# Performance work log

Hardware: AMD Instinct MI355X
Metric: run time of the kernel (lower is better)

The kernel has to match this reference:

```python
import jax, jax.numpy as jnp
import numpy as np

MARGIN = 0.35


def setup_inputs() -> dict:
    key = jax.random.key(0)
    k1, k2 = jax.random.split(key)
    N, D = 8192, 512
    inp = jax.random.normal(k1, (N, D), dtype=jnp.float32)
    label = jax.random.randint(k2, (N,), 0, D, dtype=jnp.int64)
    return {"input": inp, "label": label}


def reference(input, label):
    N = input.shape[0]
    # Faithful to the torch code: squared-norm terms use L2-normalized input,
    # but the -2*x@x.T cross term uses the UNnormalized input (original quirk).
    x_norm = input / jnp.linalg.norm(input, axis=1, keepdims=True)
    sq = jnp.sum(x_norm * x_norm, axis=1, keepdims=True)  # [N,1]
    dist = sq + sq.T - 2.0 * (input @ input.T)            # [N,N]
    mask = label[:, None] == label[None, :]               # same-label mask
    neg_inf = jnp.array(-jnp.inf, dist.dtype)
    pos_inf = jnp.array(jnp.inf, dist.dtype)
    # hardest positive (max over same-label), hardest negative (min over diff-label)
    positive_part = jnp.max(jnp.where(mask, dist, neg_inf), axis=1)
    negative_part = jnp.min(jnp.where(mask, pos_inf, dist), axis=1)
    triplet = jnp.mean(jnp.maximum(positive_part - negative_part + MARGIN, 0.0))
    # cross entropy: input are logits, label class indices
    logz = jax.nn.logsumexp(input, axis=1)
    true_logit = jnp.take_along_axis(input, label[:, None].astype(jnp.int32), axis=1)[:, 0]
    ce = jnp.mean(logz - true_logit)
    return triplet + ce
```

## Files before the change

kernel.cpp:

```cpp
#include <hip/hip_runtime.h>
#include <hip/hip_bf16.h>
#include <stdint.h>

#define N_ROWS 8192
#define DIM 512
#define NLAB 512
#define MARGIN_F 0.35f
#define NBLK 64
#define NPURE 1953
#define NDIAG 127
#define NTILE (NPURE + NDIAG)
#define ROWSTAT_BLOCKS (N_ROWS / 4)

typedef __attribute__((ext_vector_type(4))) float floatx4;
typedef __attribute__((ext_vector_type(8))) __bf16 bf16x8;

__device__ __forceinline__ unsigned enc_f(float f) {
    unsigned u = __float_as_uint(f);
    return (u & 0x80000000u) ? ~u : (u | 0x80000000u);
}
__device__ __forceinline__ float dec_f(unsigned e) {
    unsigned u = (e & 0x80000000u) ? (e ^ 0x80000000u) : ~e;
    return __uint_as_float(u);
}

__device__ __forceinline__ void load_lds16(const void* g, void* l) {
    __builtin_amdgcn_global_load_lds((__attribute__((address_space(1))) void*)(void*)g,
                                     (__attribute__((address_space(3))) void*)l, 16, 0, 0);
}

__global__ __launch_bounds__(512) void histscan_kernel(const int* __restrict__ label,
                                                       int* __restrict__ offsetArr,
                                                       int* __restrict__ cnt,
                                                       float* __restrict__ out) {
    __shared__ int h[NLAB];
    __shared__ int sc[NLAB];
    int t = threadIdx.x;
    h[t] = 0;
    __syncthreads();
    for (int i = t; i < N_ROWS; i += 512) atomicAdd(&h[label[i]], 1);
    __syncthreads();
    int v = h[t];
    sc[t] = v;
    __syncthreads();
    for (int d = 1; d < NLAB; d <<= 1) {
        int add = (t >= d) ? sc[t - d] : 0;
        __syncthreads();
        sc[t] += add;
        __syncthreads();
    }
    offsetArr[t] = sc[t] - v;
    cnt[t] = 0;
    if (t == 0) out[0] = 0.f;
}

__global__ __launch_bounds__(256) void rowstats_kernel(const float* __restrict__ x,
                                                       const int* __restrict__ label,
                                                       const int* __restrict__ offsetArr,
                                                       int* __restrict__ cnt,
                                                       __bf16* __restrict__ abf,
                                                       int* __restrict__ sortedLabel,
                                                       float* __restrict__ cePartial,
                                                       unsigned* __restrict__ minEnc,
                                                       unsigned* __restrict__ maxEnc) {
    int gid = blockIdx.x * 256 + threadIdx.x;
    if (gid < N_ROWS) { minEnc[gid] = 0xFFFFFFFFu; maxEnc[gid] = 0u; }

    int w = threadIdx.x >> 6;
    int row = blockIdx.x * 4 + w;
    int l = threadIdx.x & 63;
    const float* xr = x + (size_t)row * DIM;
    float4 v0 = ((const float4*)xr)[2 * l];
    float4 v1 = ((const float4*)xr)[2 * l + 1];
    float vals[8] = {v0.x, v0.y, v0.z, v0.w, v1.x, v1.y, v1.z, v1.w};

    float mx = vals[0];
#pragma unroll
    for (int i = 1; i < 8; i++) mx = fmaxf(mx, vals[i]);
#pragma unroll
    for (int s = 1; s < 64; s <<= 1) mx = fmaxf(mx, __shfl_xor(mx, s, 64));

    float se = 0.f;
#pragma unroll
    for (int i = 0; i < 8; i++) se += expf(vals[i] - mx);
#pragma unroll
    for (int s = 1; s < 64; s <<= 1) se += __shfl_xor(se, s, 64);

    int pos = 0;
    if (l == 0) {
        int lab = label[row];
        pos = offsetArr[lab] + atomicAdd(&cnt[lab], 1);
        sortedLabel[pos] = lab;
    }
    pos = __shfl(pos, 0, 64);

    unsigned hp[4];
#pragma unroll
    for (int i = 0; i < 4; i++) {
        unsigned u0 = __float_as_uint(vals[2 * i]);
        u0 += 0x7FFFu + ((u0 >> 16) & 1u);
        unsigned u1 = __float_as_uint(vals[2 * i + 1]);
        u1 += 0x7FFFu + ((u1 >> 16) & 1u);
        hp[i] = (u0 >> 16) | (u1 & 0xFFFF0000u);
    }
    ((uint4*)(abf + (size_t)pos * DIM))[l] = make_uint4(hp[0], hp[1], hp[2], hp[3]);

    __shared__ float wsum[4];
    if (l == 0) {
        float tl = xr[label[row]];
        wsum[w] = mx + logf(se) - tl;
    }
    __syncthreads();
    if (threadIdx.x == 0)
        cePartial[blockIdx.x] = wsum[0] + wsum[1] + wsum[2] + wsum[3];
}

__global__ __launch_bounds__(256, 4) void gemm_kernel(const __bf16* __restrict__ A,
                                                      const int* __restrict__ sortedLabel,
                                                      unsigned* __restrict__ minEnc,
                                                      unsigned* __restrict__ maxEnc) {
    __shared__ __bf16 As[128 * 64];
    __shared__ __bf16 Bs[128 * 64];
    __shared__ float redA[128][2], redB[128][2];

    int b = blockIdx.x;
    bool diag = (b < NDIAG);
    int bi, bj;
    if (diag) {
        bi = (b < 64) ? b : (b - 63);
        bj = (b < 64) ? b : (b - 64);
    } else {
        int p = b - NDIAG;
        int ci = (int)((sqrtf(8.0f * (float)p + 1.0f) - 1.0f) * 0.5f);
        while ((ci + 1) * (ci + 2) / 2 <= p) ci++;
        while (ci * (ci + 1) / 2 > p) ci--;
        bj = p - ci * (ci + 1) / 2;
        bi = ci + 2;
    }
    int ibase = bi * 128, jbase = bj * 128;

    int t = threadIdx.x;
    int w = t >> 6, l = t & 63;
    int wm = w >> 1, wn = w & 1;
    int q = l >> 4, lm = l & 15;

    floatx4 acc[4][4];
#pragma unroll
    for (int a = 0; a < 4; a++)
#pragma unroll
        for (int c = 0; c < 4; c++) acc[a][c] = (floatx4)0.f;

    for (int kk = 0; kk < 8; kk++) {
        int k0 = kk * 64;
#pragma unroll
        for (int i2 = 0; i2 < 4; i2++) {
            int s = i2 * 256 + t;
            int r = s >> 3;
            int cg = (s & 7) ^ (r & 7);
            load_lds16(A + (size_t)(ibase + r) * DIM + k0 + cg * 8, As + s * 8);
            load_lds16(A + (size_t)(jbase + r) * DIM + k0 + cg * 8, Bs + s * 8);
        }
        __syncthreads();

#pragma unroll
        for (int ks = 0; ks < 2; ks++) {
            bf16x8 af[4], bfv[4];
#pragma unroll
            for (int tm = 0; tm < 4; tm++) {
                int R = wm * 64 + tm * 16 + lm;
                af[tm] = *(const bf16x8*)(As + R * 64 + (((ks * 4 + q) ^ (R & 7)) * 8));
            }
#pragma unroll
            for (int tn = 0; tn < 4; tn++) {
                int R = wn * 64 + tn * 16 + lm;
                bfv[tn] = *(const bf16x8*)(Bs + R * 64 + (((ks * 4 + q) ^ (R & 7)) * 8));
            }
#pragma unroll
            for (int tm = 0; tm < 4; tm++)
#pragma unroll
                for (int tn = 0; tn < 4; tn++)
                    acc[tm][tn] = __builtin_amdgcn_mfma_f32_16x16x32_bf16(af[tm], bfv[tn], acc[tm][tn], 0, 0, 0);
        }
        __syncthreads();
    }

    const float INF = __builtin_inff();

    if (!diag) {
        float mxJ[4];
#pragma unroll
        for (int tn = 0; tn < 4; tn++) mxJ[tn] = -INF;
#pragma unroll
        for (int tm = 0; tm < 4; tm++) {
#pragma unroll
            for (int r = 0; r < 4; r++) {
                int row_l = wm * 64 + tm * 16 + q * 4 + r;
                float mxI = -INF;
#pragma unroll
                for (int tn = 0; tn < 4; tn++) {
                    float v = acc[tm][tn][r];
                    mxI = fmaxf(mxI, v);
                    mxJ[tn] = fmaxf(mxJ[tn], v);
                }
#pragma unroll
                for (int s = 1; s < 16; s <<= 1)
                    mxI = fmaxf(mxI, __shfl_xor(mxI, s, 64));
                if (lm == 0) redA[row_l][wn] = mxI;
            }
        }
#pragma unroll
        for (int tn = 0; tn < 4; tn++) {
#pragma unroll
            for (int s = 16; s < 64; s <<= 1)
                mxJ[tn] = fmaxf(mxJ[tn], __shfl_xor(mxJ[tn], s, 64));
            if (q == 0) redB[wn * 64 + tn * 16 + lm][wm] = mxJ[tn];
        }
        __syncthreads();
        if (t < 128) {
            atomicMax(&maxEnc[ibase + t], enc_f(fmaxf(redA[t][0], redA[t][1])));
            atomicMax(&maxEnc[jbase + t], enc_f(fmaxf(redB[t][0], redB[t][1])));
        }
    } else {
        int* labi = (int*)As;
        int* labj = labi + 128;
        float (*redImn)[2] = (float (*)[2])(labj + 128);
        float (*redJmn)[2] = redImn + 128;
        if (t < 128) labi[t] = sortedLabel[ibase + t];
        else labj[t - 128] = sortedLabel[jbase + t - 128];
        __syncthreads();

        int jlab[4];
#pragma unroll
        for (int tn = 0; tn < 4; tn++) jlab[tn] = labj[wn * 64 + tn * 16 + lm];

        float mnJ[4], mxJ[4];
#pragma unroll
        for (int tn = 0; tn < 4; tn++) { mnJ[tn] = INF; mxJ[tn] = -INF; }

#pragma unroll
        for (int tm = 0; tm < 4; tm++) {
#pragma unroll
            for (int r = 0; r < 4; r++) {
                int row_l = wm * 64 + tm * 16 + q * 4 + r;
                int il = labi[row_l];
                float mnI = INF, mxI = -INF;
#pragma unroll
                for (int tn = 0; tn < 4; tn++) {
                    float v = acc[tm][tn][r];
                    bool same = (jlab[tn] == il);
                    float vs = same ? v : INF;
                    float vd = same ? -INF : v;
                    mnI = fminf(mnI, vs);
                    mxI = fmaxf(mxI, vd);
                    mnJ[tn] = fminf(mnJ[tn], vs);
                    mxJ[tn] = fmaxf(mxJ[tn], vd);
                }
#pragma unroll
                for (int s = 1; s < 16; s <<= 1) {
                    mnI = fminf(mnI, __shfl_xor(mnI, s, 64));
                    mxI = fmaxf(mxI, __shfl_xor(mxI, s, 64));
                }
                if (lm == 0) { redImn[row_l][wn] = mnI; redA[row_l][wn] = mxI; }
            }
        }
#pragma unroll
        for (int tn = 0; tn < 4; tn++) {
#pragma unroll
            for (int s = 16; s < 64; s <<= 1) {
                mnJ[tn] = fminf(mnJ[tn], __shfl_xor(mnJ[tn], s, 64));
                mxJ[tn] = fmaxf(mxJ[tn], __shfl_xor(mxJ[tn], s, 64));
            }
            if (q == 0) {
                int col_l = wn * 64 + tn * 16 + lm;
                redJmn[col_l][wm] = mnJ[tn];
                redB[col_l][wm] = mxJ[tn];
            }
        }
        __syncthreads();
        if (t < 128) {
            atomicMin(&minEnc[ibase + t], enc_f(fminf(redImn[t][0], redImn[t][1])));
            atomicMax(&maxEnc[ibase + t], enc_f(fmaxf(redA[t][0], redA[t][1])));
            atomicMin(&minEnc[jbase + t], enc_f(fminf(redJmn[t][0], redJmn[t][1])));
            atomicMax(&maxEnc[jbase + t], enc_f(fmaxf(redB[t][0], redB[t][1])));
        }
    }
}

__global__ __launch_bounds__(256) void finalize_kernel(const unsigned* __restrict__ minEnc,
                                                       const unsigned* __restrict__ maxEnc,
                                                       const float* __restrict__ cePartial,
                                                       float* __restrict__ out) {
    int gid = blockIdx.x * 256 + threadIdx.x;
    float mn = dec_f(minEnc[gid]);
    float mxv = dec_f(maxEnc[gid]);
    float s = fmaxf(2.0f * (mxv - mn) + MARGIN_F, 0.f);
    if (gid < ROWSTAT_BLOCKS) s += cePartial[gid];
#pragma unroll
    for (int sh = 1; sh < 64; sh <<= 1) s += __shfl_xor(s, sh, 64);
    __shared__ float red[4];
    int w = threadIdx.x >> 6, l = threadIdx.x & 63;
    if (l == 0) red[w] = s;
    __syncthreads();
    if (threadIdx.x == 0)
        atomicAdd(out, (red[0] + red[1] + red[2] + red[3]) * (1.0f / (float)N_ROWS));
}

extern "C" void kernel_launch(void* const* d_in, const int* in_sizes, int n_in,
                              void* d_out, int out_size, void* d_ws, size_t ws_size,
                              hipStream_t stream) {
    const float* x = (const float*)d_in[0];
    const int* label = (const int*)d_in[1];
    float* out = (float*)d_out;

    char* ws = (char*)d_ws;
    __bf16* abf = (__bf16*)ws;
    char* p = ws + (size_t)N_ROWS * DIM * 2;
    unsigned* minEnc = (unsigned*)p;            p += N_ROWS * 4;
    unsigned* maxEnc = (unsigned*)p;            p += N_ROWS * 4;
    float* cePartial = (float*)p;               p += ROWSTAT_BLOCKS * 4;
    int* offsetArr = (int*)p;                   p += NLAB * 4;
    int* cnt = (int*)p;                         p += NLAB * 4;
    int* sortedLabel = (int*)p;                 p += N_ROWS * 4;

    histscan_kernel<<<1, 512, 0, stream>>>(label, offsetArr, cnt, out);
    rowstats_kernel<<<ROWSTAT_BLOCKS, 256, 0, stream>>>(x, label, offsetArr, cnt, abf,
                                                        sortedLabel, cePartial, minEnc, maxEnc);
    gemm_kernel<<<NTILE, 256, 0, stream>>>(abf, sortedLabel, minEnc, maxEnc);
    finalize_kernel<<<32, 256, 0, stream>>>(minEnc, maxEnc, cePartial, out);
}
```

Measured before the change: 125.9 us.

## Switch distance GEMM from bf16 to fp8 with scaled 16x16x128 MFMA

Rowstats now quantizes input rows to fp8 e4m3 instead of bf16, and the GEMM kernel uses the f8f6f4 scaled MFMA with K=128 per instruction, so there are half as many K iterations. LDS tiles hold 128 bytes per row, keeping the same XOR swizzle. This halves the global and LDS traffic and doubles matrix throughput per instruction. The trade-off is that fp8 precision can distort the hardest positive/negative distances and move the loss outside tolerance.

```diff
diff --git a/kernel.cpp b/kernel.cpp
--- a/kernel.cpp
+++ b/kernel.cpp
@@ -13,7 +13,7 @@
 #define ROWSTAT_BLOCKS (N_ROWS / 4)
 
 typedef __attribute__((ext_vector_type(4))) float floatx4;
-typedef __attribute__((ext_vector_type(8))) __bf16 bf16x8;
+typedef __attribute__((ext_vector_type(8))) int intx8;
 
 __device__ __forceinline__ unsigned enc_f(float f) {
     unsigned u = __float_as_uint(f);
@@ -58,7 +58,7 @@
                                                        const int* __restrict__ label,
                                                        const int* __restrict__ offsetArr,
                                                        int* __restrict__ cnt,
-                                                       __bf16* __restrict__ abf,
+                                                       unsigned char* __restrict__ a8,
                                                        int* __restrict__ sortedLabel,
                                                        float* __restrict__ cePartial,
                                                        unsigned* __restrict__ minEnc,
@@ -94,16 +94,11 @@
     }
     pos = __shfl(pos, 0, 64);
 
-    unsigned hp[4];
-#pragma unroll
-    for (int i = 0; i < 4; i++) {
-        unsigned u0 = __float_as_uint(vals[2 * i]);
-        u0 += 0x7FFFu + ((u0 >> 16) & 1u);
-        unsigned u1 = __float_as_uint(vals[2 * i + 1]);
-        u1 += 0x7FFFu + ((u1 >> 16) & 1u);
-        hp[i] = (u0 >> 16) | (u1 & 0xFFFF0000u);
-    }
-    ((uint4*)(abf + (size_t)pos * DIM))[l] = make_uint4(hp[0], hp[1], hp[2], hp[3]);
+    int w0 = __builtin_amdgcn_cvt_pk_fp8_f32(vals[0], vals[1], 0, false);
+    w0 = __builtin_amdgcn_cvt_pk_fp8_f32(vals[2], vals[3], w0, true);
+    int w1 = __builtin_amdgcn_cvt_pk_fp8_f32(vals[4], vals[5], 0, false);
+    w1 = __builtin_amdgcn_cvt_pk_fp8_f32(vals[6], vals[7], w1, true);
+    ((uint2*)(a8 + (size_t)pos * DIM))[l] = make_uint2((unsigned)w0, (unsigned)w1);
 
     __shared__ float wsum[4];
     if (l == 0) {
@@ -115,12 +110,12 @@
         cePartial[blockIdx.x] = wsum[0] + wsum[1] + wsum[2] + wsum[3];
 }
 
-__global__ __launch_bounds__(256, 4) void gemm_kernel(const __bf16* __restrict__ A,
+__global__ __launch_bounds__(256, 4) void gemm_kernel(const unsigned char* __restrict__ A,
                                                       const int* __restrict__ sortedLabel,
                                                       unsigned* __restrict__ minEnc,
                                                       unsigned* __restrict__ maxEnc) {
-    __shared__ __bf16 As[128 * 64];
-    __shared__ __bf16 Bs[128 * 64];
+    __shared__ unsigned char As[128 * 128];
+    __shared__ unsigned char Bs[128 * 128];
     __shared__ float redA[128][2], redB[128][2];
 
     int b = blockIdx.x;
@@ -150,36 +145,45 @@
 #pragma unroll
         for (int c = 0; c < 4; c++) acc[a][c] = (floatx4)0.f;
 
-    for (int kk = 0; kk < 8; kk++) {
-        int k0 = kk * 64;
+    for (int kk = 0; kk < 4; kk++) {
+        int k0 = kk * 128;
 #pragma unroll
         for (int i2 = 0; i2 < 4; i2++) {
             int s = i2 * 256 + t;
             int r = s >> 3;
             int cg = (s & 7) ^ (r & 7);
-            load_lds16(A + (size_t)(ibase + r) * DIM + k0 + cg * 8, As + s * 8);
-            load_lds16(A + (size_t)(jbase + r) * DIM + k0 + cg * 8, Bs + s * 8);
-        }
-        __syncthreads();
-
-#pragma unroll
-        for (int ks = 0; ks < 2; ks++) {
-            bf16x8 af[4], bfv[4];
-#pragma unroll
-            for (int tm = 0; tm < 4; tm++) {
-                int R = wm * 64 + tm * 16 + lm;
-                af[tm] = *(const bf16x8*)(As + R * 64 + (((ks * 4 + q) ^ (R & 7)) * 8));
-            }
-#pragma unroll
-            for (int tn = 0; tn < 4; tn++) {
-                int R = wn * 64 + tn * 16 + lm;
-                bfv[tn] = *(const bf16x8*)(Bs + R * 64 + (((ks * 4 + q) ^ (R & 7)) * 8));
-            }
-#pragma unroll
-            for (int tm = 0; tm < 4; tm++)
-#pragma unroll
-                for (int tn = 0; tn < 4; tn++)
-                    acc[tm][tn] = __builtin_amdgcn_mfma_f32_16x16x32_bf16(af[tm], bfv[tn], acc[tm][tn], 0, 0, 0);
+            load_lds16(A + (size_t)(ibase + r) * DIM + k0 + cg * 16, As + s * 16);
+            load_lds16(A + (size_t)(jbase + r) * DIM + k0 + cg * 16, Bs + s * 16);
+        }
+        __syncthreads();
+
+        intx8 bfv[4];
+#pragma unroll
+        for (int tn = 0; tn < 4; tn++) {
+            int R = wn * 64 + tn * 16 + lm;
+            const int4* rowp = (const int4*)(Bs + R * 128);
+            int4 lo = rowp[(2 * q) ^ (R & 7)];
+            int4 hi = rowp[(2 * q + 1) ^ (R & 7)];
+            intx8 v;
+            v[0] = lo.x; v[1] = lo.y; v[2] = lo.z; v[3] = lo.w;
+            v[4] = hi.x; v[5] = hi.y; v[6] = hi.z; v[7] = hi.w;
+            bfv[tn] = v;
+        }
+#pragma unroll
+        for (int tm = 0; tm < 4; tm++) {
+            int R = wm * 64 + tm * 16 + lm;
+            const int4* rowp = (const int4*)(As + R * 128);
+            int4 lo = rowp[(2 * q) ^ (R & 7)];
+            int4 hi = rowp[(2 * q + 1) ^ (R & 7)];
+            intx8 af;
+            af[0] = lo.x; af[1] = lo.y; af[2] = lo.z; af[3] = lo.w;
+            af[4] = hi.x; af[5] = hi.y; af[6] = hi.z; af[7] = hi.w;
+#pragma unroll
+            for (int tn = 0; tn < 4; tn++)
+                acc[tm][tn] = __builtin_amdgcn_mfma_scale_f32_16x16x128_f8f6f4(
+                    af, bfv[tn], acc[tm][tn], 0, 0,
+                    0, 0x7F7F7F7F,
+                    0, 0x7F7F7F7F);
         }
         __syncthreads();
     }
@@ -313,8 +317,8 @@
     float* out = (float*)d_out;
 
     char* ws = (char*)d_ws;
-    __bf16* abf = (__bf16*)ws;
-    char* p = ws + (size_t)N_ROWS * DIM * 2;
+    unsigned char* a8 = (unsigned char*)ws;
+    char* p = ws + (size_t)N_ROWS * DIM;
     unsigned* minEnc = (unsigned*)p;            p += N_ROWS * 4;
     unsigned* maxEnc = (unsigned*)p;            p += N_ROWS * 4;
     float* cePartial = (float*)p;               p += ROWSTAT_BLOCKS * 4;
@@ -323,8 +327,8 @@
     int* sortedLabel = (int*)p;                 p += N_ROWS * 4;
 
     histscan_kernel<<<1, 512, 0, stream>>>(label, offsetArr, cnt, out);
-    rowstats_kernel<<<ROWSTAT_BLOCKS, 256, 0, stream>>>(x, label, offsetArr, cnt, abf,
+    rowstats_kernel<<<ROWSTAT_BLOCKS, 256, 0, stream>>>(x, label, offsetArr, cnt, a8,
                                                         sortedLabel, cePartial, minEnc, maxEnc);
-    gemm_kernel<<<NTILE, 256, 0, stream>>>(abf, sortedLabel, minEnc, maxEnc);
+    gemm_kernel<<<NTILE, 256, 0, stream>>>(a8, sortedLabel, minEnc, maxEnc);
     finalize_kernel<<<32, 256, 0, stream>>>(minEnc, maxEnc, cePartial, out);
 }
```

After: 127.9 us. No clear change (+1.6%).
